# Performance work log

Measured on AMD Instinct MI355X. Metric: run time of the kernel, lower is better.

Reference implementation:

```python
import jax, jax.numpy as jnp
import numpy as np

LN_EPS = 1e-3   # keras LayerNormalization default epsilon
EPS = 1e-5      # module's self.eps
QB = 128.0      # 2**(bits-1) with bits=8


def ste_round(x):
    # straight-through round: forward = round(x), backward = identity
    return x + jax.lax.stop_gradient(jnp.round(x) - x)


def setup_inputs() -> dict:
    key = jax.random.key(0)
    k1, k2 = jax.random.split(key)
    x = jax.random.normal(k1, (4, 8192, 1024), dtype=jnp.float32)
    weight = jax.random.normal(k2, (1024, 1024), dtype=jnp.float32) * 0.02
    ln_gamma = jnp.ones((1024,), dtype=jnp.float32)
    ln_beta = jnp.zeros((1024,), dtype=jnp.float32)
    return {"x": x, "weight": weight, "ln_gamma": ln_gamma, "ln_beta": ln_beta}


def reference(x, weight, ln_gamma, ln_beta):
    # LayerNorm over last axis (keras defaults: eps=1e-3, learnable scale/center)
    mu = jnp.mean(x, axis=-1, keepdims=True)
    var = jnp.var(x, axis=-1, keepdims=True)
    xn = (x - mu) * jax.lax.rsqrt(var + LN_EPS) * ln_gamma + ln_beta

    # 1.58-bit weight ternarization with STE round
    beta = jnp.mean(jnp.abs(weight))                     # per-tensor scale
    w_q = jnp.clip(ste_round(weight / (beta + EPS)), -1.0, 1.0)

    # activation quantization (flg_before_linear=True branch)
    gamma = jnp.max(jnp.abs(xn))                         # per-tensor absmax
    xq = jnp.clip(xn * QB / gamma, -QB + EPS, QB - EPS)

    # quantized matmul + fused rescale
    y = jnp.einsum('bsd,du->bsu', xq, w_q)
    return y * (gamma * beta / QB)
```

## Files before the change

### kernel.cpp

```cpp
#include <hip/hip_runtime.h>
#include <stdint.h>


#define M_ROWS 32768
#define KDIM 1024
#define NDIM 1024

typedef int v4i  __attribute__((ext_vector_type(4)));
typedef int v16i __attribute__((ext_vector_type(16)));

__global__ __launch_bounds__(256) void absum_k(const float* __restrict__ w,
                                               float* __restrict__ partials) {
    int idx = blockIdx.x * 256 + threadIdx.x;
    float4 v = ((const float4*)w)[idx];
    float s = fabsf(v.x) + fabsf(v.y) + fabsf(v.z) + fabsf(v.w);
    #pragma unroll
    for (int o = 32; o; o >>= 1) s += __shfl_xor(s, o);
    __shared__ float p[4];
    if ((threadIdx.x & 63) == 0) p[threadIdx.x >> 6] = s;
    __syncthreads();
    if (threadIdx.x == 0) partials[blockIdx.x] = p[0] + p[1] + p[2] + p[3];
}

__global__ __launch_bounds__(256) void quant_k(const float* __restrict__ w,
                                               const float* __restrict__ partials,
                                               char* __restrict__ wqP,
                                               float* __restrict__ wsum) {
    int t = threadIdx.x;
    float s = partials[t] + partials[t + 256] + partials[t + 512] + partials[t + 768];
    #pragma unroll
    for (int o = 32; o; o >>= 1) s += __shfl_xor(s, o);
    __shared__ float ps[4];
    if ((t & 63) == 0) ps[t >> 6] = s;
    __syncthreads();
    float total = ps[0] + ps[1] + ps[2] + ps[3];
    if (blockIdx.x == 0 && t == 0) wsum[0] = total;
    float beta = total * (1.0f / 1048576.0f);
    float inv  = 1.0f / (beta + 1e-5f);

    __shared__ char sT[64 * 80];
    int k0 = (blockIdx.x >> 4) * 64, n0 = (blockIdx.x & 15) * 64;
    int n_l = t & 63;
    #pragma unroll
    for (int r = 0; r < 16; ++r) {
        int k_l = (t >> 6) * 16 + r;
        float q = rintf(w[(size_t)(k0 + k_l) * NDIM + n0 + n_l] * inv);
        q = fminf(1.0f, fmaxf(-1.0f, q));
        sT[n_l * 80 + k_l] = (char)(int)q;
    }
    __syncthreads();
    int nn = t >> 2, c = t & 3;
    v4i val = *(const v4i*)&sT[nn * 80 + c * 16];
    int n = n0 + nn, k = k0 + c * 16;
    int idx = ((n >> 5) * 32 + (k >> 5)) * 64 + (n & 31) + ((k >> 4) & 1) * 32;
    *(v4i*)&wqP[(size_t)idx * 16] = val;
}

__global__ __launch_bounds__(256, 2) void ln_gemm_k(const float* __restrict__ x,
                                                    const float* __restrict__ g,
                                                    const float* __restrict__ bln,
                                                    const char* __restrict__ wqP,
                                                    const float* __restrict__ wsum,
                                                    float* __restrict__ out) {
    __shared__ char  sA[64 * 1024];
    __shared__ float sScl[64];

    int t = threadIdx.x;
    int w = t >> 6, lane = t & 63;
    int half = lane >> 5, l31 = lane & 31;
    int bm0 = blockIdx.x * 64;

    float4 g4[4], b4[4];
    #pragma unroll
    for (int j = 0; j < 4; ++j) {
        g4[j] = ((const float4*)g)[lane * 4 + j];
        b4[j] = ((const float4*)bln)[lane * 4 + j];
    }
    #pragma unroll 1
    for (int rr = 0; rr < 16; ++rr) {
        int row = w * 16 + rr;
        const float4* xr = (const float4*)(x + ((size_t)(bm0 + row) << 10));
        float4 v0 = xr[lane * 4], v1 = xr[lane * 4 + 1], v2 = xr[lane * 4 + 2], v3 = xr[lane * 4 + 3];
        float s  = v0.x + v0.y + v0.z + v0.w + v1.x + v1.y + v1.z + v1.w
                 + v2.x + v2.y + v2.z + v2.w + v3.x + v3.y + v3.z + v3.w;
        float ss = v0.x*v0.x + v0.y*v0.y + v0.z*v0.z + v0.w*v0.w
                 + v1.x*v1.x + v1.y*v1.y + v1.z*v1.z + v1.w*v1.w
                 + v2.x*v2.x + v2.y*v2.y + v2.z*v2.z + v2.w*v2.w
                 + v3.x*v3.x + v3.y*v3.y + v3.z*v3.z + v3.w*v3.w;
        #pragma unroll
        for (int o = 32; o; o >>= 1) { s += __shfl_xor(s, o); ss += __shfl_xor(ss, o); }
        float mu  = s * (1.0f / 1024.0f);
        float var = ss * (1.0f / 1024.0f) - mu * mu;
        float rs  = rsqrtf(var + 1e-3f);
        float xn[16];
        float4 vv[4] = {v0, v1, v2, v3};
        float mx = 0.f;
        #pragma unroll
        for (int j = 0; j < 4; ++j) {
            xn[4*j+0] = (vv[j].x - mu) * rs * g4[j].x + b4[j].x;
            xn[4*j+1] = (vv[j].y - mu) * rs * g4[j].y + b4[j].y;
            xn[4*j+2] = (vv[j].z - mu) * rs * g4[j].z + b4[j].z;
            xn[4*j+3] = (vv[j].w - mu) * rs * g4[j].w + b4[j].w;
            #pragma unroll
            for (int e = 0; e < 4; ++e) mx = fmaxf(mx, fabsf(xn[4*j+e]));
        }
        #pragma unroll
        for (int o = 32; o; o >>= 1) mx = fmaxf(mx, __shfl_xor(mx, o));
        mx = fmaxf(mx, 1e-20f);
        float inv = 127.0f / mx;
        if (lane == 0) sScl[row] = mx * (1.0f / 127.0f);
        int qw[4];
        #pragma unroll
        for (int j = 0; j < 4; ++j) {
            int b0 = (int)rintf(xn[4*j+0] * inv) & 255;
            int b1 = (int)rintf(xn[4*j+1] * inv) & 255;
            int b2 = (int)rintf(xn[4*j+2] * inv) & 255;
            int b3 = (int)rintf(xn[4*j+3] * inv) & 255;
            qw[j] = b0 | (b1 << 8) | (b2 << 16) | (b3 << 24);
        }
        v4i qv; qv[0] = qw[0]; qv[1] = qw[1]; qv[2] = qw[2]; qv[3] = qw[3];
        int mf = row >> 5, r31 = row & 31;
        int slot = r31 ^ (lane & 7);
        *(v4i*)&sA[(((mf * 64 + lane) * 32) + slot) * 16] = qv;
    }
    __syncthreads();

    float beta = wsum[0] * (1.0f / 1048576.0f);
    const v4i* wp = (const v4i*)wqP;

    #pragma unroll 1
    for (int p = 0; p < 2; ++p) {
        int nbB = p * 16 + w * 4;
        v16i acc[2][4] = {};
        v4i a0[2], a1[2], b0[4], b1[4];

        #define LA(dst, S) do { \
            int u_ = 2 * (S) + half; \
            int o_ = ((u_ * 32) + (l31 ^ (u_ & 7))) * 16; \
            dst[0] = *(const v4i*)&sA[o_]; \
            dst[1] = *(const v4i*)&sA[o_ + 32768]; \
        } while (0)
        #define LB(dst, S) do { \
            _Pragma("unroll") \
            for (int j_ = 0; j_ < 4; ++j_) \
                dst[j_] = wp[(size_t)(((nbB + j_) * 32 + (S)) * 64) + lane]; \
        } while (0)

        LB(b0, 0); LB(b1, 1); LA(a0, 0); LA(a1, 1);
        #pragma unroll 1
        for (int s = 0; s < 32; s += 2) {
            #pragma unroll
            for (int mf = 0; mf < 2; ++mf)
                #pragma unroll
                for (int j = 0; j < 4; ++j)
                    acc[mf][j] = __builtin_amdgcn_mfma_i32_32x32x32_i8(a0[mf], b0[j], acc[mf][j], 0, 0, 0);
            if (s + 2 < 32) { LB(b0, s + 2); LA(a0, s + 2); }
            #pragma unroll
            for (int mf = 0; mf < 2; ++mf)
                #pragma unroll
                for (int j = 0; j < 4; ++j)
                    acc[mf][j] = __builtin_amdgcn_mfma_i32_32x32x32_i8(a1[mf], b1[j], acc[mf][j], 0, 0, 0);
            if (s + 3 < 32) { LB(b1, s + 3); LA(a1, s + 3); }
        }
        #undef LA
        #undef LB

        #pragma unroll
        for (int mf = 0; mf < 2; ++mf) {
            #pragma unroll
            for (int r = 0; r < 16; ++r) {
                int rloc = mf * 32 + (r & 3) + 8 * (r >> 2) + 4 * half;
                float sc = sScl[rloc] * beta;
                size_t o = (size_t)(bm0 + rloc) * NDIM + p * 512 + w * 128 + l31;
                out[o]      = (float)acc[0 + mf][0][r] * sc;
                out[o + 32] = (float)acc[0 + mf][1][r] * sc;
                out[o + 64] = (float)acc[0 + mf][2][r] * sc;
                out[o + 96] = (float)acc[0 + mf][3][r] * sc;
            }
        }
    }
}

extern "C" void kernel_launch(void* const* d_in, const int* in_sizes, int n_in,
                              void* d_out, int out_size, void* d_ws, size_t ws_size,
                              hipStream_t stream) {
    const float* x        = (const float*)d_in[0];
    const float* weight   = (const float*)d_in[1];
    const float* ln_gamma = (const float*)d_in[2];
    const float* ln_beta  = (const float*)d_in[3];
    float* out = (float*)d_out;

    float* wsum     = (float*)d_ws;
    float* partials = (float*)((char*)d_ws + 4096);
    char*  wqP      = (char*)d_ws + (1u << 18);

    absum_k<<<1024, 256, 0, stream>>>(weight, partials);
    quant_k<<<256, 256, 0, stream>>>(weight, partials, wqP, wsum);
    ln_gemm_k<<<M_ROWS / 64, 256, 0, stream>>>(x, ln_gamma, ln_beta, wqP, wsum, out);
}
```

Baseline: 283.9 us.

## Use 512-thread blocks with narrower per-wave GEMM tiles and coalesced LN loads

The fused LayerNorm+int8 GEMM kernel now runs 8 waves per 64-row block instead of 4. Each wave normalises 8 rows and computes a 64x32 output strip per pass over 4 passes, where it used to compute a 64x128 tile over 2 passes. x loads now use a lane-strided float4 pattern for coalescing, and the quantized bytes are written to LDS as char4 in the existing swizzled layout. The aim is more latency hiding and occupancy at the cost of more LDS A-fragment reads per MFMA and less register reuse of B fragments.

After: 335.3 us. +18.1%, slower.

```diff
diff --git a/kernel.cpp b/kernel.cpp
--- a/kernel.cpp
+++ b/kernel.cpp
@@ -56,7 +56,7 @@
     *(v4i*)&wqP[(size_t)idx * 16] = val;
 }
 
-__global__ __launch_bounds__(256, 2) void ln_gemm_k(const float* __restrict__ x,
+__global__ __launch_bounds__(512, 4) void ln_gemm_k(const float* __restrict__ x,
                                                     const float* __restrict__ g,
                                                     const float* __restrict__ bln,
                                                     const char* __restrict__ wqP,
@@ -73,14 +73,14 @@
     float4 g4[4], b4[4];
     #pragma unroll
     for (int j = 0; j < 4; ++j) {
-        g4[j] = ((const float4*)g)[lane * 4 + j];
-        b4[j] = ((const float4*)bln)[lane * 4 + j];
+        g4[j] = ((const float4*)g)[lane + 64 * j];
+        b4[j] = ((const float4*)bln)[lane + 64 * j];
     }
-    #pragma unroll 1
-    for (int rr = 0; rr < 16; ++rr) {
-        int row = w * 16 + rr;
+    #pragma unroll 2
+    for (int rr = 0; rr < 8; ++rr) {
+        int row = w * 8 + rr;
         const float4* xr = (const float4*)(x + ((size_t)(bm0 + row) << 10));
-        float4 v0 = xr[lane * 4], v1 = xr[lane * 4 + 1], v2 = xr[lane * 4 + 2], v3 = xr[lane * 4 + 3];
+        float4 v0 = xr[lane], v1 = xr[lane + 64], v2 = xr[lane + 128], v3 = xr[lane + 192];
         float s  = v0.x + v0.y + v0.z + v0.w + v1.x + v1.y + v1.z + v1.w
                  + v2.x + v2.y + v2.z + v2.w + v3.x + v3.y + v3.z + v3.w;
         float ss = v0.x*v0.x + v0.y*v0.y + v0.z*v0.z + v0.w*v0.w
@@ -93,92 +93,87 @@
         float var = ss * (1.0f / 1024.0f) - mu * mu;
         float rs  = rsqrtf(var + 1e-3f);
         float xn[16];
-        float4 vv[4] = {v0, v1, v2, v3};
         float mx = 0.f;
-        #pragma unroll
-        for (int j = 0; j < 4; ++j) {
-            xn[4*j+0] = (vv[j].x - mu) * rs * g4[j].x + b4[j].x;
-            xn[4*j+1] = (vv[j].y - mu) * rs * g4[j].y + b4[j].y;
-            xn[4*j+2] = (vv[j].z - mu) * rs * g4[j].z + b4[j].z;
-            xn[4*j+3] = (vv[j].w - mu) * rs * g4[j].w + b4[j].w;
-            #pragma unroll
-            for (int e = 0; e < 4; ++e) mx = fmaxf(mx, fabsf(xn[4*j+e]));
-        }
+        #define LNQ(j, vv) do { \
+            xn[4*(j)+0] = (vv.x - mu) * rs * g4[j].x + b4[j].x; \
+            xn[4*(j)+1] = (vv.y - mu) * rs * g4[j].y + b4[j].y; \
+            xn[4*(j)+2] = (vv.z - mu) * rs * g4[j].z + b4[j].z; \
+            xn[4*(j)+3] = (vv.w - mu) * rs * g4[j].w + b4[j].w; \
+            mx = fmaxf(mx, fmaxf(fmaxf(fabsf(xn[4*(j)+0]), fabsf(xn[4*(j)+1])), \
+                                 fmaxf(fabsf(xn[4*(j)+2]), fabsf(xn[4*(j)+3])))); \
+        } while (0)
+        LNQ(0, v0); LNQ(1, v1); LNQ(2, v2); LNQ(3, v3);
+        #undef LNQ
         #pragma unroll
         for (int o = 32; o; o >>= 1) mx = fmaxf(mx, __shfl_xor(mx, o));
         mx = fmaxf(mx, 1e-20f);
         float inv = 127.0f / mx;
         if (lane == 0) sScl[row] = mx * (1.0f / 127.0f);
-        int qw[4];
+        int mf = row >> 5, r31 = row & 31;
         #pragma unroll
         for (int j = 0; j < 4; ++j) {
-            int b0 = (int)rintf(xn[4*j+0] * inv) & 255;
-            int b1 = (int)rintf(xn[4*j+1] * inv) & 255;
-            int b2 = (int)rintf(xn[4*j+2] * inv) & 255;
-            int b3 = (int)rintf(xn[4*j+3] * inv) & 255;
-            qw[j] = b0 | (b1 << 8) | (b2 << 16) | (b3 << 24);
+            char4 c4;
+            c4.x = (char)(int)rintf(xn[4*j+0] * inv);
+            c4.y = (char)(int)rintf(xn[4*j+1] * inv);
+            c4.z = (char)(int)rintf(xn[4*j+2] * inv);
+            c4.w = (char)(int)rintf(xn[4*j+3] * inv);
+            int u    = (lane >> 2) + 16 * j;
+            int slot = r31 ^ (u & 7);
+            *(char4*)&sA[mf * 32768 + (u * 32 + slot) * 16 + (lane & 3) * 4] = c4;
         }
-        v4i qv; qv[0] = qw[0]; qv[1] = qw[1]; qv[2] = qw[2]; qv[3] = qw[3];
-        int mf = row >> 5, r31 = row & 31;
-        int slot = r31 ^ (lane & 7);
-        *(v4i*)&sA[(((mf * 64 + lane) * 32) + slot) * 16] = qv;
     }
     __syncthreads();
 
     float beta = wsum[0] * (1.0f / 1048576.0f);
     const v4i* wp = (const v4i*)wqP;
 
+    #define LA(dst, S) do { \
+        int u_ = 2 * (S) + half; \
+        int o_ = ((u_ * 32) + (l31 ^ (u_ & 7))) * 16; \
+        dst[0] = *(const v4i*)&sA[o_]; \
+        dst[1] = *(const v4i*)&sA[o_ + 32768]; \
+    } while (0)
+
     #pragma unroll 1
-    for (int p = 0; p < 2; ++p) {
-        int nbB = p * 16 + w * 4;
-        v16i acc[2][4] = {};
-        v4i a0[2], a1[2], b0[4], b1[4];
+    for (int p = 0; p < 4; ++p) {
+        int nb = p * 8 + w;
+        size_t fb = (size_t)nb * 32 * 64;
+        v16i acc0 = {}, acc1 = {};
+        v4i a0[2], a1[2], a2[2], a3[2], b0, b1, b2, b3;
 
-        #define LA(dst, S) do { \
-            int u_ = 2 * (S) + half; \
-            int o_ = ((u_ * 32) + (l31 ^ (u_ & 7))) * 16; \
-            dst[0] = *(const v4i*)&sA[o_]; \
-            dst[1] = *(const v4i*)&sA[o_ + 32768]; \
-        } while (0)
-        #define LB(dst, S) do { \
-            _Pragma("unroll") \
-            for (int j_ = 0; j_ < 4; ++j_) \
-                dst[j_] = wp[(size_t)(((nbB + j_) * 32 + (S)) * 64) + lane]; \
-        } while (0)
+        b0 = wp[fb + 0 * 64 + lane];
+        b1 = wp[fb + 1 * 64 + lane];
+        b2 = wp[fb + 2 * 64 + lane];
+        b3 = wp[fb + 3 * 64 + lane];
+        LA(a0, 0); LA(a1, 1); LA(a2, 2); LA(a3, 3);
 
-        LB(b0, 0); LB(b1, 1); LA(a0, 0); LA(a1, 1);
         #pragma unroll 1
-        for (int s = 0; s < 32; s += 2) {
-            #pragma unroll
-            for (int mf = 0; mf < 2; ++mf)
-                #pragma unroll
-                for (int j = 0; j < 4; ++j)
-                    acc[mf][j] = __builtin_amdgcn_mfma_i32_32x32x32_i8(a0[mf], b0[j], acc[mf][j], 0, 0, 0);
-            if (s + 2 < 32) { LB(b0, s + 2); LA(a0, s + 2); }
-            #pragma unroll
-            for (int mf = 0; mf < 2; ++mf)
-                #pragma unroll
-                for (int j = 0; j < 4; ++j)
-                    acc[mf][j] = __builtin_amdgcn_mfma_i32_32x32x32_i8(a1[mf], b1[j], acc[mf][j], 0, 0, 0);
-            if (s + 3 < 32) { LB(b1, s + 3); LA(a1, s + 3); }
+        for (int s = 0; s < 32; s += 4) {
+            acc0 = __builtin_amdgcn_mfma_i32_32x32x32_i8(a0[0], b0, acc0, 0, 0, 0);
+            acc1 = __builtin_amdgcn_mfma_i32_32x32x32_i8(a0[1], b0, acc1, 0, 0, 0);
+            if (s + 4 < 32) { b0 = wp[fb + (size_t)(s + 4) * 64 + lane]; LA(a0, s + 4); }
+            acc0 = __builtin_amdgcn_mfma_i32_32x32x32_i8(a1[0], b1, acc0, 0, 0, 0);
+            acc1 = __builtin_amdgcn_mfma_i32_32x32x32_i8(a1[1], b1, acc1, 0, 0, 0);
+            if (s + 5 < 32) { b1 = wp[fb + (size_t)(s + 5) * 64 + lane]; LA(a1, s + 5); }
+            acc0 = __builtin_amdgcn_mfma_i32_32x32x32_i8(a2[0], b2, acc0, 0, 0, 0);
+            acc1 = __builtin_amdgcn_mfma_i32_32x32x32_i8(a2[1], b2, acc1, 0, 0, 0);
+            if (s + 6 < 32) { b2 = wp[fb + (size_t)(s + 6) * 64 + lane]; LA(a2, s + 6); }
+            acc0 = __builtin_amdgcn_mfma_i32_32x32x32_i8(a3[0], b3, acc0, 0, 0, 0);
+            acc1 = __builtin_amdgcn_mfma_i32_32x32x32_i8(a3[1], b3, acc1, 0, 0, 0);
+            if (s + 7 < 32) { b3 = wp[fb + (size_t)(s + 7) * 64 + lane]; LA(a3, s + 7); }
         }
-        #undef LA
-        #undef LB
 
         #pragma unroll
-        for (int mf = 0; mf < 2; ++mf) {
-            #pragma unroll
-            for (int r = 0; r < 16; ++r) {
-                int rloc = mf * 32 + (r & 3) + 8 * (r >> 2) + 4 * half;
-                float sc = sScl[rloc] * beta;
-                size_t o = (size_t)(bm0 + rloc) * NDIM + p * 512 + w * 128 + l31;
-                out[o]      = (float)acc[0 + mf][0][r] * sc;
-                out[o + 32] = (float)acc[0 + mf][1][r] * sc;
-                out[o + 64] = (float)acc[0 + mf][2][r] * sc;
-                out[o + 96] = (float)acc[0 + mf][3][r] * sc;
-            }
+        for (int r = 0; r < 16; ++r) {
+            int rl = (r & 3) + 8 * (r >> 2) + 4 * half;
+            float sc0 = sScl[rl] * beta;
+            float sc1 = sScl[32 + rl] * beta;
+            size_t o = (size_t)(bm0 + rl) * NDIM + nb * 32 + l31;
+            out[o]                      = (float)acc0[r] * sc0;
+            out[o + (size_t)32 * NDIM]  = (float)acc1[r] * sc1;
         }
     }
+    #undef LA
 }
 
 extern "C" void kernel_launch(void* const* d_in, const int* in_sizes, int n_in,
@@ -196,5 +191,5 @@
 
     absum_k<<<1024, 256, 0, stream>>>(weight, partials);
     quant_k<<<256, 256, 0, stream>>>(weight, partials, wqP, wsum);
-    ln_gemm_k<<<M_ROWS / 64, 256, 0, stream>>>(x, ln_gamma, ln_beta, wqP, wsum, out);
+    ln_gemm_k<<<M_ROWS / 64, 512, 0, stream>>>(x, ln_gamma, ln_beta, wqP, wsum, out);
 }
```
